# Kernel tuning notes

Hardware: AMD Instinct MI355X
Metric: run time of the kernel (lower is better)

The kernel has to match this reference:

```python
import jax, jax.numpy as jnp
import numpy as np
import math

B, T, S, D, H = 2, 1024, 1024, 1024, 16
DH = D // H


def setup_inputs() -> dict:
    key = jax.random.key(0)
    ks = jax.random.split(key, 13)
    scale = 1.0 / math.sqrt(D)
    inp = {
        "q": jax.random.normal(ks[0], (B, T, D), jnp.float32),
        "k": jax.random.normal(ks[1], (B, S, D), jnp.float32),
        "v": jax.random.normal(ks[2], (B, S, D), jnp.float32),
        # causal mask: True means masked
        "attn_mask": jnp.broadcast_to(
            jnp.triu(jnp.ones((T, S), jnp.bool_), k=1)[None, None], (B, 1, T, S)
        ),
        "attn_bias": jax.random.normal(ks[3], (B, H, T, S), jnp.float32),
        "Wq": jax.random.normal(ks[4], (D, D), jnp.float32) * scale,
        "bq": jnp.zeros((D,), jnp.float32),
        "Wk": jax.random.normal(ks[5], (D, D), jnp.float32) * scale,
        "bk": jnp.zeros((D,), jnp.float32),
        "Wv": jax.random.normal(ks[6], (D, D), jnp.float32) * scale,
        "bv": jnp.zeros((D,), jnp.float32),
        "Wo": jax.random.normal(ks[7], (D, D), jnp.float32) * scale,
        "bo": jnp.zeros((D,), jnp.float32),
        "bias_scale": jnp.asarray(0.5, jnp.float32),
    }
    return inp


def reference(q, k, v, attn_mask, attn_bias, Wq, bq, Wk, bk, Wv, bv, Wo, bo, bias_scale):
    # projections (torch Linear convention: x @ W.T + b), split heads
    qh = (q @ Wq.T + bq).reshape(B, T, H, DH)   # (B,T,H,DH)
    kh = (k @ Wk.T + bk).reshape(B, S, H, DH)
    vh = (v @ Wv.T + bv).reshape(B, S, H, DH)

    scores = jnp.einsum("bthd,bshd->bhts", qh, kh) / math.sqrt(DH)  # (B,H,T,S)
    scores = jnp.clip(scores, -80.0, 80.0)
    scores = jnp.where(attn_mask, -jnp.inf, scores)  # mask broadcasts over H
    attn = jax.nn.softmax(scores, axis=-1)

    # post-softmax multiplicative bias + renormalize
    scale = 1.0 + bias_scale * jnp.tanh(attn_bias)
    attn = attn * jnp.maximum(scale, 1e-9)
    attn = attn / (jnp.sum(attn, axis=-1, keepdims=True) + 1e-9)

    # dropout p=0.0 (eval) -> identity
    out = jnp.einsum("bhts,bshd->bthd", attn, vh).reshape(B, T, D)
    out = out @ Wo.T + bo
    return out, attn
```

## Files before the change

kernel.cpp:

```cpp
#include <hip/hip_runtime.h>
#include <hip/hip_bf16.h>
#include <math.h>

#define BB 2
#define TT 1024
#define SS 1024
#define DD 1024
#define HH 16
#define DH 64

typedef __attribute__((ext_vector_type(8))) short bf16x8;
typedef __attribute__((ext_vector_type(4))) float f32x4;
typedef unsigned short ushort_t;

#define AS3(p) ((__attribute__((address_space(3))) unsigned int*)(p))
#define AS1(p) ((const __attribute__((address_space(1))) unsigned int*)(p))

__device__ __forceinline__ unsigned short f2b(float f) {
    union { float f; unsigned u; } x; x.f = f;
    unsigned r = x.u + 0x7FFFu + ((x.u >> 16) & 1u);
    return (unsigned short)(r >> 16);
}

__global__ __launch_bounds__(256) void cvt3_kernel(
    const float* __restrict__ a, const float* __restrict__ b, const float* __restrict__ c,
    ushort_t* __restrict__ oa, ushort_t* __restrict__ ob, ushort_t* __restrict__ oc)
{
    const float* src = (blockIdx.y == 0) ? a : (blockIdx.y == 1) ? b : c;
    ushort_t* dst    = (blockIdx.y == 0) ? oa : (blockIdx.y == 1) ? ob : oc;
    size_t i = ((size_t)blockIdx.x * 256 + threadIdx.x) * 8;
    float4 v0 = *(const float4*)&src[i];
    float4 v1 = *(const float4*)&src[i + 4];
    uint4 o;
    o.x = f2b(v0.x) | ((unsigned)f2b(v0.y) << 16);
    o.y = f2b(v0.z) | ((unsigned)f2b(v0.w) << 16);
    o.z = f2b(v1.x) | ((unsigned)f2b(v1.y) << 16);
    o.w = f2b(v1.z) | ((unsigned)f2b(v1.w) << 16);
    *(uint4*)&dst[i] = o;
}

__global__ __launch_bounds__(256) void cvt4_kernel(
    const float* __restrict__ a, const float* __restrict__ b,
    const float* __restrict__ c, const float* __restrict__ d,
    ushort_t* __restrict__ oa, ushort_t* __restrict__ ob,
    ushort_t* __restrict__ oc, ushort_t* __restrict__ od)
{
    const float* src = (blockIdx.y == 0) ? a : (blockIdx.y == 1) ? b : (blockIdx.y == 2) ? c : d;
    ushort_t* dst    = (blockIdx.y == 0) ? oa : (blockIdx.y == 1) ? ob : (blockIdx.y == 2) ? oc : od;
    size_t i = ((size_t)blockIdx.x * 256 + threadIdx.x) * 8;
    float4 v0 = *(const float4*)&src[i];
    float4 v1 = *(const float4*)&src[i + 4];
    uint4 o;
    o.x = f2b(v0.x) | ((unsigned)f2b(v0.y) << 16);
    o.y = f2b(v0.z) | ((unsigned)f2b(v0.w) << 16);
    o.z = f2b(v1.x) | ((unsigned)f2b(v1.y) << 16);
    o.w = f2b(v1.z) | ((unsigned)f2b(v1.w) << 16);
    *(uint4*)&dst[i] = o;
}

__device__ __forceinline__ void gemm128_mainloop(
    const ushort_t* __restrict__ A,
    const ushort_t* __restrict__ Bw,
    int K, ushort_t* Asm, ushort_t* Bsm, f32x4 acc[4][4])
{
    const int tid = threadIdx.x;
    const int wave = tid >> 6, lane = tid & 63;
    const int sr = lane >> 2;
    const int gc = (lane & 3) ^ ((lane >> 3) & 3);
    const int l15 = lane & 15, q = lane >> 4;
    const int mblk = (wave >> 1) * 64, nblk = (wave & 1) * 64;

    for (int k0 = 0; k0 < K; k0 += 32) {
        #pragma unroll
        for (int o = 0; o < 2; o++) {
            int r0 = (wave * 2 + o) * 16;
            __builtin_amdgcn_global_load_lds(AS1(A + (size_t)(r0 + sr) * K + k0 + gc * 8),
                                             AS3(Asm + r0 * 32), 16, 0, 0);
            __builtin_amdgcn_global_load_lds(AS1(Bw + (size_t)(r0 + sr) * K + k0 + gc * 8),
                                             AS3(Bsm + r0 * 32), 16, 0, 0);
        }
        __syncthreads();

        bf16x8 av[4], bv[4];
        #pragma unroll
        for (int mi = 0; mi < 4; mi++) {
            int r = mblk + mi * 16 + l15;
            av[mi] = *(const bf16x8*)&Asm[r * 32 + (q ^ ((r >> 1) & 3)) * 8];
        }
        #pragma unroll
        for (int ni = 0; ni < 4; ni++) {
            int r = nblk + ni * 16 + l15;
            bv[ni] = *(const bf16x8*)&Bsm[r * 32 + (q ^ ((r >> 1) & 3)) * 8];
        }
        #pragma unroll
        for (int mi = 0; mi < 4; mi++)
            #pragma unroll
            for (int ni = 0; ni < 4; ni++)
                acc[mi][ni] = __builtin_amdgcn_mfma_f32_16x16x32_bf16(av[mi], bv[ni], acc[mi][ni], 0, 0, 0);
        __syncthreads();
    }
}

__global__ __launch_bounds__(256) void proj_gemm(
    const ushort_t* __restrict__ qb, const ushort_t* __restrict__ kb, const ushort_t* __restrict__ vb,
    const ushort_t* __restrict__ Wqb, const ushort_t* __restrict__ Wkb, const ushort_t* __restrict__ Wvb,
    const float* __restrict__ bq, const float* __restrict__ bk, const float* __restrict__ bv,
    ushort_t* __restrict__ qh, ushort_t* __restrict__ kh, ushort_t* __restrict__ vh)
{
    __shared__ ushort_t Asm[128 * 32];
    __shared__ ushort_t Bsm[128 * 32];
    const int z = blockIdx.z;
    const ushort_t* A = (z == 0) ? qb : (z == 1) ? kb : vb;
    const ushort_t* W = (z == 0) ? Wqb : (z == 1) ? Wkb : Wvb;
    const float* bias = (z == 0) ? bq : (z == 1) ? bk : bv;
    ushort_t* Y = (z == 0) ? qh : (z == 1) ? kh : vh;

    const int bm = blockIdx.y * 128, bn = blockIdx.x * 128;
    f32x4 acc[4][4];
    #pragma unroll
    for (int i = 0; i < 4; i++)
        #pragma unroll
        for (int j = 0; j < 4; j++) acc[i][j] = (f32x4)(0.f);

    gemm128_mainloop(A + (size_t)bm * DD, W + (size_t)bn * DD, DD, Asm, Bsm, acc);

    const int lane = threadIdx.x & 63, wave = threadIdx.x >> 6;
    const int mblk = (wave >> 1) * 64, nblk = (wave & 1) * 64;
    const int l15 = lane & 15, q = lane >> 4;
    #pragma unroll
    for (int mi = 0; mi < 4; mi++) {
        #pragma unroll
        for (int ni = 0; ni < 4; ni++) {
            int col = bn + nblk + ni * 16 + l15;
            float bcol = bias[col];
            #pragma unroll
            for (int r = 0; r < 4; r++) {
                int row = bm + mblk + mi * 16 + q * 4 + r;
                Y[(size_t)row * DD + col] = f2b(acc[mi][ni][r] + bcol);
            }
        }
    }
}

__global__ __launch_bounds__(256) void oproj_gemm(
    const ushort_t* __restrict__ A, const ushort_t* __restrict__ W,
    const float* __restrict__ bias, float* __restrict__ Y)
{
    __shared__ ushort_t Asm[128 * 32];
    __shared__ ushort_t Bsm[128 * 32];
    const int bm = blockIdx.y * 128, bn = blockIdx.x * 128;
    f32x4 acc[4][4];
    #pragma unroll
    for (int i = 0; i < 4; i++)
        #pragma unroll
        for (int j = 0; j < 4; j++) acc[i][j] = (f32x4)(0.f);

    gemm128_mainloop(A + (size_t)bm * DD, W + (size_t)bn * DD, DD, Asm, Bsm, acc);

    const int lane = threadIdx.x & 63, wave = threadIdx.x >> 6;
    const int mblk = (wave >> 1) * 64, nblk = (wave & 1) * 64;
    const int l15 = lane & 15, q = lane >> 4;
    #pragma unroll
    for (int mi = 0; mi < 4; mi++) {
        #pragma unroll
        for (int ni = 0; ni < 4; ni++) {
            int col = bn + nblk + ni * 16 + l15;
            float bcol = bias[col];
            #pragma unroll
            for (int r = 0; r < 4; r++) {
                int row = bm + mblk + mi * 16 + q * 4 + r;
                Y[(size_t)row * DD + col] = acc[mi][ni][r] + bcol;
            }
        }
    }
}

__global__ __launch_bounds__(256) void transpose_v(
    const ushort_t* __restrict__ vh, ushort_t* __restrict__ vT)
{
    __shared__ ushort_t Ls[64][72];
    const int s0 = blockIdx.x * 64;
    const int bh = blockIdx.y;
    const int b = bh >> 4, h = bh & 15;
    const int tid = threadIdx.x;
    const int r = tid >> 2, c16 = (tid & 3) * 16;

    const ushort_t* src = &vh[((size_t)(b * SS + s0 + r) * HH + h) * DH + c16];
    uint4 u0 = *(const uint4*)src;
    uint4 u1 = *(const uint4*)(src + 8);
    ushort_t tmp[16];
    *(uint4*)&tmp[0] = u0; *(uint4*)&tmp[8] = u1;
    #pragma unroll
    for (int j = 0; j < 16; j++) Ls[c16 + j][r] = tmp[j];
    __syncthreads();

    const int dh = r;
    uint4 w0 = *(const uint4*)&Ls[dh][c16];
    uint4 w1 = *(const uint4*)&Ls[dh][c16 + 8];
    ushort_t* dst = &vT[((size_t)bh * DH + dh) * SS + s0 + c16];
    *(uint4*)dst = w0;
    *(uint4*)(dst + 8) = w1;
}

__global__ __launch_bounds__(256) void scores_mfma(
    const ushort_t* __restrict__ qh, const ushort_t* __restrict__ kh,
    float* __restrict__ attn)
{
    __shared__ ushort_t Qs[128 * 64];
    __shared__ ushort_t Ks[128 * 64];

    int idx = blockIdx.x, ti = 0;
    while (idx >= ti + 1) { idx -= ti + 1; ti++; }
    const int si = idx;
    const int bh = blockIdx.y;
    const int b = bh >> 4, h = bh & 15;
    const int t0 = ti * 128, s0 = si * 128;

    const int tid = threadIdx.x;
    const int wave = tid >> 6, lane = tid & 63;
    const int sr8 = lane >> 3;
    const int gc8 = (lane & 7) ^ sr8;

    #pragma unroll
    for (int o = 0; o < 4; o++) {
        int r0 = (wave * 4 + o) * 8;
        int r = r0 + sr8;
        __builtin_amdgcn_global_load_lds(
            AS1(qh + ((size_t)(b * TT + t0 + r) * HH + h) * DH + gc8 * 8),
            AS3(Qs + r0 * 64), 16, 0, 0);
        __builtin_amdgcn_global_load_lds(
            AS1(kh + ((size_t)(b * SS + s0 + r) * HH + h) * DH + gc8 * 8),
            AS3(Ks + r0 * 64), 16, 0, 0);
    }
    __syncthreads();

    const int l15 = lane & 15, q = lane >> 4;
    const int tblk = (wave >> 1) * 64, sblk = (wave & 1) * 64;
    f32x4 acc[4][4];
    #pragma unroll
    for (int i = 0; i < 4; i++)
        #pragma unroll
        for (int j = 0; j < 4; j++) acc[i][j] = (f32x4)(0.f);

    #pragma unroll
    for (int ks = 0; ks < 2; ks++) {
        bf16x8 av[4], bv[4];
        #pragma unroll
        for (int mi = 0; mi < 4; mi++) {
            int r = tblk + mi * 16 + l15;
            av[mi] = *(const bf16x8*)&Qs[r * 64 + ((ks * 4 + q) ^ (r & 7)) * 8];
        }
        #pragma unroll
        for (int ni = 0; ni < 4; ni++) {
            int r = sblk + ni * 16 + l15;
            bv[ni] = *(const bf16x8*)&Ks[r * 64 + ((ks * 4 + q) ^ (r & 7)) * 8];
        }
        #pragma unroll
        for (int mi = 0; mi < 4; mi++)
            #pragma unroll
            for (int ni = 0; ni < 4; ni++)
                acc[mi][ni] = __builtin_amdgcn_mfma_f32_16x16x32_bf16(av[mi], bv[ni], acc[mi][ni], 0, 0, 0);
    }

    #pragma unroll
    for (int mi = 0; mi < 4; mi++) {
        #pragma unroll
        for (int ni = 0; ni < 4; ni++) {
            int scol = s0 + sblk + ni * 16 + l15;
            #pragma unroll
            for (int r = 0; r < 4; r++) {
                int t = t0 + tblk + mi * 16 + q * 4 + r;
                float v = acc[mi][ni][r] * 0.125f;
                v = fminf(fmaxf(v, -80.f), 80.f);
                attn[((size_t)bh * TT + t) * SS + scol] = v;
            }
        }
    }
}

__global__ __launch_bounds__(256) void softmax_bias_kernel(
    const float* __restrict__ attn_bias, const float* __restrict__ bias_scale_p,
    float* __restrict__ attn)
{
    const int bid = blockIdx.x;
    const int t = bid & (TT - 1);
    const int tid = threadIdx.x;
    const int s0 = tid * 4;

    float* row = attn + (size_t)bid * SS;
    const float* brow = attn_bias + (size_t)bid * SS;

    __shared__ float red[256];

    float v0 = -INFINITY, v1 = -INFINITY, v2 = -INFINITY, v3 = -INFINITY;
    if (s0 <= t) {
        float4 rv = *(const float4*)&row[s0];
        v0 = rv.x;
        v1 = (s0 + 1 <= t) ? rv.y : -INFINITY;
        v2 = (s0 + 2 <= t) ? rv.z : -INFINITY;
        v3 = (s0 + 3 <= t) ? rv.w : -INFINITY;
    }
    float lmax = fmaxf(fmaxf(v0, v1), fmaxf(v2, v3));
    red[tid] = lmax;
    __syncthreads();
    for (int off = 128; off > 0; off >>= 1) {
        if (tid < off) red[tid] = fmaxf(red[tid], red[tid + off]);
        __syncthreads();
    }
    const float m = red[0];
    __syncthreads();

    float p0 = (v0 > -INFINITY) ? __expf(v0 - m) : 0.f;
    float p1 = (v1 > -INFINITY) ? __expf(v1 - m) : 0.f;
    float p2 = (v2 > -INFINITY) ? __expf(v2 - m) : 0.f;
    float p3 = (v3 > -INFINITY) ? __expf(v3 - m) : 0.f;
    red[tid] = p0 + p1 + p2 + p3;
    __syncthreads();
    for (int off = 128; off > 0; off >>= 1) {
        if (tid < off) red[tid] += red[tid + off];
        __syncthreads();
    }
    const float inv = 1.f / red[0];
    __syncthreads();

    const float bscale = bias_scale_p[0];
    float w0 = 0.f, w1 = 0.f, w2 = 0.f, w3 = 0.f;
    if (s0 <= t) {
        float4 bv = *(const float4*)&brow[s0];
        float e0 = __expf(-2.f * fabsf(bv.x));
        float e1 = __expf(-2.f * fabsf(bv.y));
        float e2 = __expf(-2.f * fabsf(bv.z));
        float e3 = __expf(-2.f * fabsf(bv.w));
        float t0 = copysignf((1.f - e0) / (1.f + e0), bv.x);
        float t1 = copysignf((1.f - e1) / (1.f + e1), bv.y);
        float t2 = copysignf((1.f - e2) / (1.f + e2), bv.z);
        float t3 = copysignf((1.f - e3) / (1.f + e3), bv.w);
        w0 = p0 * inv * fmaxf(1.f + bscale * t0, 1e-9f);
        w1 = p1 * inv * fmaxf(1.f + bscale * t1, 1e-9f);
        w2 = p2 * inv * fmaxf(1.f + bscale * t2, 1e-9f);
        w3 = p3 * inv * fmaxf(1.f + bscale * t3, 1e-9f);
    }
    red[tid] = w0 + w1 + w2 + w3;
    __syncthreads();
    for (int off = 128; off > 0; off >>= 1) {
        if (tid < off) red[tid] += red[tid + off];
        __syncthreads();
    }
    const float inv2 = 1.f / (red[0] + 1e-9f);

    float4 o;
    o.x = w0 * inv2; o.y = w1 * inv2; o.z = w2 * inv2; o.w = w3 * inv2;
    *(float4*)&row[s0] = o;
}

__global__ __launch_bounds__(256) void av_mfma(
    const float* __restrict__ attn, const ushort_t* __restrict__ vT,
    ushort_t* __restrict__ ao)
{
    __shared__ ushort_t Asm[64 * 32];
    __shared__ ushort_t Vsm[64 * 32];

    const int tb = blockIdx.x;
    const int bh = blockIdx.y;
    const int b = bh >> 4, h = bh & 15;
    const int t0 = tb * 64;
    const int nsteps = (tb + 1) * 2;

    const int tid = threadIdx.x;
    const int wave = tid >> 6, lane = tid & 63;
    const int ar = tid >> 2, aq = tid & 3;
    const int aslot = aq ^ ((ar >> 1) & 3);
    const int vsr = lane >> 2;
    const int vgc = (lane & 3) ^ ((lane >> 3) & 3);
    const int l15 = lane & 15, q = lane >> 4;

    f32x4 acc[4];
    #pragma unroll
    for (int i = 0; i < 4; i++) acc[i] = (f32x4)(0.f);

    for (int st = 0; st < nsteps; st++) {
        const int s0 = st * 32;
        {
            const float* src = &attn[((size_t)bh * TT + t0 + ar) * SS + s0 + aq * 8];
            float4 u0 = *(const float4*)src;
            float4 u1 = *(const float4*)(src + 4);
            uint4 o;
            o.x = f2b(u0.x) | ((unsigned)f2b(u0.y) << 16);
            o.y = f2b(u0.z) | ((unsigned)f2b(u0.w) << 16);
            o.z = f2b(u1.x) | ((unsigned)f2b(u1.y) << 16);
            o.w = f2b(u1.z) | ((unsigned)f2b(u1.w) << 16);
            *(uint4*)&Asm[ar * 32 + aslot * 8] = o;
        }
        {
            int r0 = wave * 16;
            __builtin_amdgcn_global_load_lds(
                AS1(vT + ((size_t)bh * DH + r0 + vsr) * SS + s0 + vgc * 8),
                AS3(Vsm + r0 * 32), 16, 0, 0);
        }
        __syncthreads();

        bf16x8 a0, bv[4];
        {
            int r = wave * 16 + l15;
            a0 = *(const bf16x8*)&Asm[r * 32 + (q ^ ((r >> 1) & 3)) * 8];
        }
        #pragma unroll
        for (int ni = 0; ni < 4; ni++) {
            int r = ni * 16 + l15;
            bv[ni] = *(const bf16x8*)&Vsm[r * 32 + (q ^ ((r >> 1) & 3)) * 8];
        }
        #pragma unroll
        for (int ni = 0; ni < 4; ni++)
            acc[ni] = __builtin_amdgcn_mfma_f32_16x16x32_bf16(a0, bv[ni], acc[ni], 0, 0, 0);
        __syncthreads();
    }

    #pragma unroll
    for (int ni = 0; ni < 4; ni++) {
        int dh = ni * 16 + l15;
        #pragma unroll
        for (int r = 0; r < 4; r++) {
            int t = t0 + wave * 16 + q * 4 + r;
            ao[(size_t)(b * TT + t) * DD + h * DH + dh] = f2b(acc[ni][r]);
        }
    }
}

extern "C" void kernel_launch(void* const* d_in, const int* in_sizes, int n_in,
                              void* d_out, int out_size, void* d_ws, size_t ws_size,
                              hipStream_t stream)
{
    const float* q   = (const float*)d_in[0];
    const float* k   = (const float*)d_in[1];
    const float* v   = (const float*)d_in[2];
    const float* attn_bias = (const float*)d_in[4];
    const float* Wq = (const float*)d_in[5];
    const float* bq = (const float*)d_in[6];
    const float* Wk = (const float*)d_in[7];
    const float* bk = (const float*)d_in[8];
    const float* Wv = (const float*)d_in[9];
    const float* bv = (const float*)d_in[10];
    const float* Wo = (const float*)d_in[11];
    const float* bo = (const float*)d_in[12];
    const float* bscale = (const float*)d_in[13];

    char* base = (char*)d_ws;
    ushort_t* qb  = (ushort_t*)(base + (0ull << 20));
    ushort_t* kb  = (ushort_t*)(base + (4ull << 20));
    ushort_t* vb  = (ushort_t*)(base + (8ull << 20));
    ushort_t* Wqb = (ushort_t*)(base + (12ull << 20));
    ushort_t* Wkb = (ushort_t*)(base + (14ull << 20));
    ushort_t* Wvb = (ushort_t*)(base + (16ull << 20));
    ushort_t* Wob = (ushort_t*)(base + (18ull << 20));
    ushort_t* qhb = (ushort_t*)(base + (20ull << 20));
    ushort_t* khb = (ushort_t*)(base + (24ull << 20));
    ushort_t* vhb = (ushort_t*)(base + (28ull << 20));
    ushort_t* vT  = qb;
    ushort_t* aob = kb;

    float* out  = (float*)d_out;
    float* attn = out + (size_t)BB * TT * DD;

    cvt3_kernel<<<dim3(1024, 3), 256, 0, stream>>>(q, k, v, qb, kb, vb);
    cvt4_kernel<<<dim3(512, 4), 256, 0, stream>>>(Wq, Wk, Wv, Wo, Wqb, Wkb, Wvb, Wob);
    proj_gemm<<<dim3(8, 16, 3), 256, 0, stream>>>(qb, kb, vb, Wqb, Wkb, Wvb,
                                                  bq, bk, bv, qhb, khb, vhb);
    transpose_v<<<dim3(16, 32), 256, 0, stream>>>(vhb, vT);
    scores_mfma<<<dim3(36, 32), 256, 0, stream>>>(qhb, khb, attn);
    softmax_bias_kernel<<<dim3(BB * HH * TT), 256, 0, stream>>>(attn_bias, bscale, attn);
    av_mfma<<<dim3(16, 32), 256, 0, stream>>>(attn, vT, aob);
    oproj_gemm<<<dim3(8, 16), 256, 0, stream>>>(aob, Wob, bo, out);
}
```

Measured before the change: 395.9 us.

## Fuse QK scores and biased softmax into a two-pass attention kernel

Replaces the separate scores GEMM kernel and the per-row softmax/bias kernel with one kernel. Each block owns 64 query rows of one head. A first pass over the causal key tiles computes running max, softmax sum and bias-weighted sum with an online rescale. A second pass recomputes QK and writes the final normalized probabilities directly, and the upper triangle is zero-filled. This removes the fp32 scores round trip through memory and the block-wide reductions, but it reads the bias twice, repeats the QK MFMAs, and runs only 512 blocks of uneven causal length.

Result: slower. 556.0 us (+40.4%).

```diff
diff --git a/kernel.cpp b/kernel.cpp
--- a/kernel.cpp
+++ b/kernel.cpp
@@ -202,155 +202,179 @@
     *(uint4*)(dst + 8) = w1;
 }
 
-__global__ __launch_bounds__(256) void scores_mfma(
+__global__ __launch_bounds__(256) void attn_fused(
     const ushort_t* __restrict__ qh, const ushort_t* __restrict__ kh,
+    const float* __restrict__ attn_bias, const float* __restrict__ bias_scale_p,
     float* __restrict__ attn)
 {
-    __shared__ ushort_t Qs[128 * 64];
-    __shared__ ushort_t Ks[128 * 64];
-
-    int idx = blockIdx.x, ti = 0;
-    while (idx >= ti + 1) { idx -= ti + 1; ti++; }
-    const int si = idx;
+    __shared__ ushort_t Ks[64 * 64];
+
+    const int ti = (int)gridDim.x - 1 - (int)blockIdx.x;
     const int bh = blockIdx.y;
     const int b = bh >> 4, h = bh & 15;
-    const int t0 = ti * 128, s0 = si * 128;
+    const int t0 = ti * 64;
+    const int nS = ti + 1;
 
     const int tid = threadIdx.x;
     const int wave = tid >> 6, lane = tid & 63;
+    const int l15 = lane & 15, q = lane >> 4;
     const int sr8 = lane >> 3;
     const int gc8 = (lane & 7) ^ sr8;
-
-    #pragma unroll
-    for (int o = 0; o < 4; o++) {
-        int r0 = (wave * 4 + o) * 8;
-        int r = r0 + sr8;
-        __builtin_amdgcn_global_load_lds(
-            AS1(qh + ((size_t)(b * TT + t0 + r) * HH + h) * DH + gc8 * 8),
-            AS3(Qs + r0 * 64), 16, 0, 0);
-        __builtin_amdgcn_global_load_lds(
-            AS1(kh + ((size_t)(b * SS + s0 + r) * HH + h) * DH + gc8 * 8),
-            AS3(Ks + r0 * 64), 16, 0, 0);
-    }
-    __syncthreads();
-
-    const int l15 = lane & 15, q = lane >> 4;
-    const int tblk = (wave >> 1) * 64, sblk = (wave & 1) * 64;
-    f32x4 acc[4][4];
-    #pragma unroll
-    for (int i = 0; i < 4; i++)
-        #pragma unroll
-        for (int j = 0; j < 4; j++) acc[i][j] = (f32x4)(0.f);
-
-    #pragma unroll
-    for (int ks = 0; ks < 2; ks++) {
-        bf16x8 av[4], bv[4];
-        #pragma unroll
-        for (int mi = 0; mi < 4; mi++) {
-            int r = tblk + mi * 16 + l15;
-            av[mi] = *(const bf16x8*)&Qs[r * 64 + ((ks * 4 + q) ^ (r & 7)) * 8];
-        }
-        #pragma unroll
-        for (int ni = 0; ni < 4; ni++) {
-            int r = sblk + ni * 16 + l15;
-            bv[ni] = *(const bf16x8*)&Ks[r * 64 + ((ks * 4 + q) ^ (r & 7)) * 8];
-        }
-        #pragma unroll
-        for (int mi = 0; mi < 4; mi++)
-            #pragma unroll
-            for (int ni = 0; ni < 4; ni++)
-                acc[mi][ni] = __builtin_amdgcn_mfma_f32_16x16x32_bf16(av[mi], bv[ni], acc[mi][ni], 0, 0, 0);
-    }
-
-    #pragma unroll
-    for (int mi = 0; mi < 4; mi++) {
-        #pragma unroll
-        for (int ni = 0; ni < 4; ni++) {
-            int scol = s0 + sblk + ni * 16 + l15;
-            #pragma unroll
-            for (int r = 0; r < 4; r++) {
-                int t = t0 + tblk + mi * 16 + q * 4 + r;
-                float v = acc[mi][ni][r] * 0.125f;
-                v = fminf(fmaxf(v, -80.f), 80.f);
-                attn[((size_t)bh * TT + t) * SS + scol] = v;
-            }
-        }
-    }
-}
-
-__global__ __launch_bounds__(256) void softmax_bias_kernel(
-    const float* __restrict__ attn_bias, const float* __restrict__ bias_scale_p,
-    float* __restrict__ attn)
-{
-    const int bid = blockIdx.x;
-    const int t = bid & (TT - 1);
-    const int tid = threadIdx.x;
-    const int s0 = tid * 4;
-
-    float* row = attn + (size_t)bid * SS;
-    const float* brow = attn_bias + (size_t)bid * SS;
-
-    __shared__ float red[256];
-
-    float v0 = -INFINITY, v1 = -INFINITY, v2 = -INFINITY, v3 = -INFINITY;
-    if (s0 <= t) {
-        float4 rv = *(const float4*)&row[s0];
-        v0 = rv.x;
-        v1 = (s0 + 1 <= t) ? rv.y : -INFINITY;
-        v2 = (s0 + 2 <= t) ? rv.z : -INFINITY;
-        v3 = (s0 + 3 <= t) ? rv.w : -INFINITY;
-    }
-    float lmax = fmaxf(fmaxf(v0, v1), fmaxf(v2, v3));
-    red[tid] = lmax;
-    __syncthreads();
-    for (int off = 128; off > 0; off >>= 1) {
-        if (tid < off) red[tid] = fmaxf(red[tid], red[tid + off]);
-        __syncthreads();
-    }
-    const float m = red[0];
-    __syncthreads();
-
-    float p0 = (v0 > -INFINITY) ? __expf(v0 - m) : 0.f;
-    float p1 = (v1 > -INFINITY) ? __expf(v1 - m) : 0.f;
-    float p2 = (v2 > -INFINITY) ? __expf(v2 - m) : 0.f;
-    float p3 = (v3 > -INFINITY) ? __expf(v3 - m) : 0.f;
-    red[tid] = p0 + p1 + p2 + p3;
-    __syncthreads();
-    for (int off = 128; off > 0; off >>= 1) {
-        if (tid < off) red[tid] += red[tid + off];
-        __syncthreads();
-    }
-    const float inv = 1.f / red[0];
-    __syncthreads();
-
     const float bscale = bias_scale_p[0];
-    float w0 = 0.f, w1 = 0.f, w2 = 0.f, w3 = 0.f;
-    if (s0 <= t) {
-        float4 bv = *(const float4*)&brow[s0];
-        float e0 = __expf(-2.f * fabsf(bv.x));
-        float e1 = __expf(-2.f * fabsf(bv.y));
-        float e2 = __expf(-2.f * fabsf(bv.z));
-        float e3 = __expf(-2.f * fabsf(bv.w));
-        float t0 = copysignf((1.f - e0) / (1.f + e0), bv.x);
-        float t1 = copysignf((1.f - e1) / (1.f + e1), bv.y);
-        float t2 = copysignf((1.f - e2) / (1.f + e2), bv.z);
-        float t3 = copysignf((1.f - e3) / (1.f + e3), bv.w);
-        w0 = p0 * inv * fmaxf(1.f + bscale * t0, 1e-9f);
-        w1 = p1 * inv * fmaxf(1.f + bscale * t1, 1e-9f);
-        w2 = p2 * inv * fmaxf(1.f + bscale * t2, 1e-9f);
-        w3 = p3 * inv * fmaxf(1.f + bscale * t3, 1e-9f);
-    }
-    red[tid] = w0 + w1 + w2 + w3;
-    __syncthreads();
-    for (int off = 128; off > 0; off >>= 1) {
-        if (tid < off) red[tid] += red[tid + off];
-        __syncthreads();
-    }
-    const float inv2 = 1.f / (red[0] + 1e-9f);
-
-    float4 o;
-    o.x = w0 * inv2; o.y = w1 * inv2; o.z = w2 * inv2; o.w = w3 * inv2;
-    *(float4*)&row[s0] = o;
+
+    for (int si = nS; si < SS / 64; si++) {
+        const int s0 = si * 64;
+        #pragma unroll
+        for (int i = 0; i < 4; i++) {
+            int row = i * 16 + (tid >> 4);
+            float4 z = make_float4(0.f, 0.f, 0.f, 0.f);
+            *(float4*)&attn[((size_t)bh * TT + t0 + row) * SS + s0 + (tid & 15) * 4] = z;
+        }
+    }
+
+    bf16x8 aq[2];
+    {
+        const int row = t0 + wave * 16 + l15;
+        const ushort_t* src = &qh[((size_t)(b * TT + row) * HH + h) * DH + q * 8];
+        aq[0] = *(const bf16x8*)src;
+        aq[1] = *(const bf16x8*)(src + 32);
+    }
+
+    const int tr = t0 + wave * 16 + q * 4;
+
+    float m[4], P[4], W[4];
+    #pragma unroll
+    for (int r = 0; r < 4; r++) { m[r] = -INFINITY; P[r] = 0.f; W[r] = 0.f; }
+
+    for (int si = 0; si < nS; si++) {
+        const int s0 = si * 64;
+        #pragma unroll
+        for (int o = 0; o < 2; o++) {
+            int r0 = wave * 16 + o * 8;
+            __builtin_amdgcn_global_load_lds(
+                AS1(kh + ((size_t)(b * SS + s0 + r0 + sr8) * HH + h) * DH + gc8 * 8),
+                AS3(Ks + r0 * 64), 16, 0, 0);
+        }
+        __syncthreads();
+
+        f32x4 acc[4];
+        #pragma unroll
+        for (int ni = 0; ni < 4; ni++) acc[ni] = (f32x4)(0.f);
+        #pragma unroll
+        for (int ks = 0; ks < 2; ks++) {
+            #pragma unroll
+            for (int ni = 0; ni < 4; ni++) {
+                int r = ni * 16 + l15;
+                bf16x8 bv = *(const bf16x8*)&Ks[r * 64 + ((ks * 4 + q) ^ (r & 7)) * 8];
+                acc[ni] = __builtin_amdgcn_mfma_f32_16x16x32_bf16(aq[ks], bv, acc[ni], 0, 0, 0);
+            }
+        }
+        __syncthreads();
+
+        float tmax[4];
+        #pragma unroll
+        for (int r = 0; r < 4; r++) tmax[r] = -INFINITY;
+        #pragma unroll
+        for (int ni = 0; ni < 4; ni++) {
+            int s = s0 + ni * 16 + l15;
+            #pragma unroll
+            for (int r = 0; r < 4; r++) {
+                float v = fminf(fmaxf(acc[ni][r] * 0.125f, -80.f), 80.f);
+                if (s <= tr + r) tmax[r] = fmaxf(tmax[r], v);
+            }
+        }
+        #pragma unroll
+        for (int off = 1; off < 16; off <<= 1) {
+            #pragma unroll
+            for (int r = 0; r < 4; r++)
+                tmax[r] = fmaxf(tmax[r], __shfl_xor(tmax[r], off));
+        }
+
+        float pP[4], pW[4];
+        #pragma unroll
+        for (int r = 0; r < 4; r++) {
+            float mn = fmaxf(m[r], tmax[r]);
+            float f = (mn == m[r]) ? 1.f : __expf(m[r] - mn);
+            P[r] *= f; W[r] *= f; m[r] = mn;
+            pP[r] = 0.f; pW[r] = 0.f;
+        }
+        #pragma unroll
+        for (int ni = 0; ni < 4; ni++) {
+            int s = s0 + ni * 16 + l15;
+            #pragma unroll
+            for (int r = 0; r < 4; r++) {
+                if (s <= tr + r) {
+                    float v = fminf(fmaxf(acc[ni][r] * 0.125f, -80.f), 80.f);
+                    float p = __expf(v - m[r]);
+                    float bvv = attn_bias[((size_t)bh * TT + tr + r) * SS + s];
+                    float e = __expf(-2.f * fabsf(bvv));
+                    float th = copysignf((1.f - e) / (1.f + e), bvv);
+                    float sc = fmaxf(1.f + bscale * th, 1e-9f);
+                    pP[r] += p;
+                    pW[r] += p * sc;
+                }
+            }
+        }
+        #pragma unroll
+        for (int off = 1; off < 16; off <<= 1) {
+            #pragma unroll
+            for (int r = 0; r < 4; r++) {
+                pP[r] += __shfl_xor(pP[r], off);
+                pW[r] += __shfl_xor(pW[r], off);
+            }
+        }
+        #pragma unroll
+        for (int r = 0; r < 4; r++) { P[r] += pP[r]; W[r] += pW[r]; }
+    }
+
+    float inv[4];
+    #pragma unroll
+    for (int r = 0; r < 4; r++) inv[r] = 1.f / (W[r] + 1e-9f * P[r]);
+
+    for (int si = 0; si < nS; si++) {
+        const int s0 = si * 64;
+        #pragma unroll
+        for (int o = 0; o < 2; o++) {
+            int r0 = wave * 16 + o * 8;
+            __builtin_amdgcn_global_load_lds(
+                AS1(kh + ((size_t)(b * SS + s0 + r0 + sr8) * HH + h) * DH + gc8 * 8),
+                AS3(Ks + r0 * 64), 16, 0, 0);
+        }
+        __syncthreads();
+
+        f32x4 acc[4];
+        #pragma unroll
+        for (int ni = 0; ni < 4; ni++) acc[ni] = (f32x4)(0.f);
+        #pragma unroll
+        for (int ks = 0; ks < 2; ks++) {
+            #pragma unroll
+            for (int ni = 0; ni < 4; ni++) {
+                int r = ni * 16 + l15;
+                bf16x8 bv = *(const bf16x8*)&Ks[r * 64 + ((ks * 4 + q) ^ (r & 7)) * 8];
+                acc[ni] = __builtin_amdgcn_mfma_f32_16x16x32_bf16(aq[ks], bv, acc[ni], 0, 0, 0);
+            }
+        }
+        __syncthreads();
+
+        #pragma unroll
+        for (int ni = 0; ni < 4; ni++) {
+            int s = s0 + ni * 16 + l15;
+            #pragma unroll
+            for (int r = 0; r < 4; r++) {
+                float res = 0.f;
+                if (s <= tr + r) {
+                    float v = fminf(fmaxf(acc[ni][r] * 0.125f, -80.f), 80.f);
+                    float p = __expf(v - m[r]);
+                    float bvv = attn_bias[((size_t)bh * TT + tr + r) * SS + s];
+                    float e = __expf(-2.f * fabsf(bvv));
+                    float th = copysignf((1.f - e) / (1.f + e), bvv);
+                    float sc = fmaxf(1.f + bscale * th, 1e-9f);
+                    res = p * sc * inv[r];
+                }
+                attn[((size_t)bh * TT + tr + r) * SS + s] = res;
+            }
+        }
+    }
 }
 
 __global__ __launch_bounds__(256) void av_mfma(
@@ -466,8 +490,7 @@
     proj_gemm<<<dim3(8, 16, 3), 256, 0, stream>>>(qb, kb, vb, Wqb, Wkb, Wvb,
                                                   bq, bk, bv, qhb, khb, vhb);
     transpose_v<<<dim3(16, 32), 256, 0, stream>>>(vhb, vT);
-    scores_mfma<<<dim3(36, 32), 256, 0, stream>>>(qhb, khb, attn);
-    softmax_bias_kernel<<<dim3(BB * HH * TT), 256, 0, stream>>>(attn_bias, bscale, attn);
+    attn_fused<<<dim3(16, 32), 256, 0, stream>>>(qhb, khb, attn_bias, bscale, attn);
     av_mfma<<<dim3(16, 32), 256, 0, stream>>>(attn, vT, aob);
     oproj_gemm<<<dim3(8, 16), 256, 0, stream>>>(aob, Wob, bo, out);
 }
```

## Process one softmax row per wavefront with shuffle reductions

Applied to the files above, without the earlier changes.

Rewrites the softmax/bias kernel so each 64-lane wavefront handles a full row, with 16 values per lane, instead of a 256-thread block per row. The three LDS tree reductions with many __syncthreads are replaced by wave-level shuffle reductions. The two normalizations are folded into one by dividing by Wn + 1e-9*P. Loads are skipped for fully masked 256-column chunks. Register use rises, and the folded normalization changes rounding slightly.

Result: faster. 374.9 us (-5.3%).

```diff
diff --git a/kernel.cpp b/kernel.cpp
--- a/kernel.cpp
+++ b/kernel.cpp
@@ -278,79 +278,80 @@
     }
 }
 
-__global__ __launch_bounds__(256) void softmax_bias_kernel(
+__global__ __launch_bounds__(256) void softmax_bias_wave(
     const float* __restrict__ attn_bias, const float* __restrict__ bias_scale_p,
     float* __restrict__ attn)
 {
-    const int bid = blockIdx.x;
-    const int t = bid & (TT - 1);
-    const int tid = threadIdx.x;
-    const int s0 = tid * 4;
-
-    float* row = attn + (size_t)bid * SS;
-    const float* brow = attn_bias + (size_t)bid * SS;
-
-    __shared__ float red[256];
-
-    float v0 = -INFINITY, v1 = -INFINITY, v2 = -INFINITY, v3 = -INFINITY;
-    if (s0 <= t) {
-        float4 rv = *(const float4*)&row[s0];
-        v0 = rv.x;
-        v1 = (s0 + 1 <= t) ? rv.y : -INFINITY;
-        v2 = (s0 + 2 <= t) ? rv.z : -INFINITY;
-        v3 = (s0 + 3 <= t) ? rv.w : -INFINITY;
-    }
-    float lmax = fmaxf(fmaxf(v0, v1), fmaxf(v2, v3));
-    red[tid] = lmax;
-    __syncthreads();
-    for (int off = 128; off > 0; off >>= 1) {
-        if (tid < off) red[tid] = fmaxf(red[tid], red[tid + off]);
-        __syncthreads();
-    }
-    const float m = red[0];
-    __syncthreads();
-
-    float p0 = (v0 > -INFINITY) ? __expf(v0 - m) : 0.f;
-    float p1 = (v1 > -INFINITY) ? __expf(v1 - m) : 0.f;
-    float p2 = (v2 > -INFINITY) ? __expf(v2 - m) : 0.f;
-    float p3 = (v3 > -INFINITY) ? __expf(v3 - m) : 0.f;
-    red[tid] = p0 + p1 + p2 + p3;
-    __syncthreads();
-    for (int off = 128; off > 0; off >>= 1) {
-        if (tid < off) red[tid] += red[tid + off];
-        __syncthreads();
-    }
-    const float inv = 1.f / red[0];
-    __syncthreads();
-
+    const int wave = threadIdx.x >> 6, lane = threadIdx.x & 63;
+    const int row = blockIdx.x * 4 + wave;
+    const int t = row & (TT - 1);
+
+    float* prow = attn + (size_t)row * SS;
+    const float* brow = attn_bias + (size_t)row * SS;
     const float bscale = bias_scale_p[0];
-    float w0 = 0.f, w1 = 0.f, w2 = 0.f, w3 = 0.f;
-    if (s0 <= t) {
-        float4 bv = *(const float4*)&brow[s0];
-        float e0 = __expf(-2.f * fabsf(bv.x));
-        float e1 = __expf(-2.f * fabsf(bv.y));
-        float e2 = __expf(-2.f * fabsf(bv.z));
-        float e3 = __expf(-2.f * fabsf(bv.w));
-        float t0 = copysignf((1.f - e0) / (1.f + e0), bv.x);
-        float t1 = copysignf((1.f - e1) / (1.f + e1), bv.y);
-        float t2 = copysignf((1.f - e2) / (1.f + e2), bv.z);
-        float t3 = copysignf((1.f - e3) / (1.f + e3), bv.w);
-        w0 = p0 * inv * fmaxf(1.f + bscale * t0, 1e-9f);
-        w1 = p1 * inv * fmaxf(1.f + bscale * t1, 1e-9f);
-        w2 = p2 * inv * fmaxf(1.f + bscale * t2, 1e-9f);
-        w3 = p3 * inv * fmaxf(1.f + bscale * t3, 1e-9f);
-    }
-    red[tid] = w0 + w1 + w2 + w3;
-    __syncthreads();
-    for (int off = 128; off > 0; off >>= 1) {
-        if (tid < off) red[tid] += red[tid + off];
-        __syncthreads();
-    }
-    const float inv2 = 1.f / (red[0] + 1e-9f);
-
-    float4 o;
-    o.x = w0 * inv2; o.y = w1 * inv2; o.z = w2 * inv2; o.w = w3 * inv2;
-    *(float4*)&row[s0] = o;
+
+    const int nc = (t >> 8) + 1;
+
+    float v[16];
+    float m = -INFINITY;
+    #pragma unroll
+    for (int c = 0; c < 4; c++) {
+        const int s0 = c * 256 + lane * 4;
+        if (c < nc) {
+            float4 rv = *(const float4*)&prow[s0];
+            v[c * 4 + 0] = (s0     <= t) ? rv.x : -INFINITY;
+            v[c * 4 + 1] = (s0 + 1 <= t) ? rv.y : -INFINITY;
+            v[c * 4 + 2] = (s0 + 2 <= t) ? rv.z : -INFINITY;
+            v[c * 4 + 3] = (s0 + 3 <= t) ? rv.w : -INFINITY;
+            m = fmaxf(m, fmaxf(fmaxf(v[c*4], v[c*4+1]), fmaxf(v[c*4+2], v[c*4+3])));
+        } else {
+            v[c * 4 + 0] = -INFINITY; v[c * 4 + 1] = -INFINITY;
+            v[c * 4 + 2] = -INFINITY; v[c * 4 + 3] = -INFINITY;
+        }
+    }
+    #pragma unroll
+    for (int off = 1; off < 64; off <<= 1)
+        m = fmaxf(m, __shfl_xor(m, off));
+
+    float w[16];
+    float P = 0.f, Wn = 0.f;
+    #pragma unroll
+    for (int c = 0; c < 4; c++) {
+        const int s0 = c * 256 + lane * 4;
+        if (c < nc) {
+            float4 bv = *(const float4*)&brow[s0];
+            float bx[4] = {bv.x, bv.y, bv.z, bv.w};
+            #pragma unroll
+            for (int j = 0; j < 4; j++) {
+                float vv = v[c * 4 + j];
+                float p = (vv > -INFINITY) ? __expf(vv - m) : 0.f;
+                float e = __expf(-2.f * fabsf(bx[j]));
+                float th = copysignf((1.f - e) / (1.f + e), bx[j]);
+                float sc = fmaxf(1.f + bscale * th, 1e-9f);
+                float ww = p * sc;
+                w[c * 4 + j] = ww;
+                P += p; Wn += ww;
+            }
+        } else {
+            w[c * 4 + 0] = 0.f; w[c * 4 + 1] = 0.f;
+            w[c * 4 + 2] = 0.f; w[c * 4 + 3] = 0.f;
+        }
+    }
+    #pragma unroll
+    for (int off = 1; off < 64; off <<= 1) {
+        P  += __shfl_xor(P, off);
+        Wn += __shfl_xor(Wn, off);
+    }
+    const float inv = 1.f / (Wn + 1e-9f * P);
+
+    #pragma unroll
+    for (int c = 0; c < 4; c++) {
+        const int s0 = c * 256 + lane * 4;
+        float4 o;
+        o.x = w[c * 4 + 0] * inv; o.y = w[c * 4 + 1] * inv;
+        o.z = w[c * 4 + 2] * inv; o.w = w[c * 4 + 3] * inv;
+        *(float4*)&prow[s0] = o;
+    }
 }
 
 __global__ __launch_bounds__(256) void av_mfma(
@@ -467,7 +468,7 @@
                                                   bq, bk, bv, qhb, khb, vhb);
     transpose_v<<<dim3(16, 32), 256, 0, stream>>>(vhb, vT);
     scores_mfma<<<dim3(36, 32), 256, 0, stream>>>(qhb, khb, attn);
-    softmax_bias_kernel<<<dim3(BB * HH * TT), 256, 0, stream>>>(attn_bias, bscale, attn);
+    softmax_bias_wave<<<dim3(8192), 256, 0, stream>>>(attn_bias, bscale, attn);
     av_mfma<<<dim3(16, 32), 256, 0, stream>>>(attn, vT, aob);
     oproj_gemm<<<dim3(8, 16), 256, 0, stream>>>(aob, Wob, bo, out);
 }
```
